# Performance work log

Measured on AMD Instinct MI355X. Metric: run time of the kernel, lower is better.

The kernel has to match this reference:

```python
import jax, jax.numpy as jnp
import numpy as np
import math

EMBED_DIM = 512
VOCAB = 96          # 95 printable ASCII + <UNK>
N_TOKENS = 16384
ALPHA = 1.5
BETA = 0.8
FRACTAL = 1.7
THETA = 0.1          # SO(4) rotation angle
LN_EPS = 1e-5        # torch LayerNorm default


def _semantic_table():
    """Faithful per-character semantic weights, L2-normalized rows. [VOCAB,4]."""
    wmap = {
        'vowels': [1.2, 0.8, 1.5, 0.9],
        'consonants': [0.9, 1.1, 0.7, 1.3],
        'digits': [1.0, 1.0, 1.0, 1.0],
        'punctuation': [0.5, 0.5, 0.8, 0.8],
        'whitespace': [0.3, 0.3, 0.3, 0.3],
        'unknown': [0.1, 0.1, 0.1, 0.1],
    }
    vocab = [chr(i) for i in range(32, 127)] + ['<UNK>']

    def cat(c):
        if c in 'aeiouAEIOU':
            return 'vowels'
        if c in 'bcdfghjklmnpqrstvwxyzBCDFGHJKLMNPQRSTVWXYZ':
            return 'consonants'
        if c in '0123456789':
            return 'digits'
        if c == ' ':
            return 'whitespace'
        if c == '<UNK>':
            return 'unknown'
        return 'punctuation'

    t = np.array([wmap[cat(c)] for c in vocab], dtype=np.float32)
    return t / np.linalg.norm(t, axis=1, keepdims=True)


def setup_inputs() -> dict:
    key = jax.random.key(0)
    k1, k2, k3, k4 = jax.random.split(key, 4)
    D, N = EMBED_DIM, N_TOKENS
    return {
        'char_idx': jax.random.randint(k1, (N,), 0, VOCAB, dtype=jnp.int32),
        'positions': jax.random.randint(k2, (N,), 0, 512, dtype=jnp.int32),
        'W': jax.random.normal(k3, (D, D), dtype=jnp.float32) * (1.0 / math.sqrt(D)),
        'b': jnp.zeros((D,), dtype=jnp.float32),
        'gamma': jnp.ones((D,), dtype=jnp.float32),
        'beta_ln': jnp.zeros((D,), dtype=jnp.float32),
        'noise': jax.random.normal(k4, (N, D), dtype=jnp.float32),  # scaled by 0.01 inside
        'sem_table': jnp.asarray(_semantic_table()),
    }


def reference(char_idx, positions, W, b, gamma, beta_ln, noise, sem_table):
    D = EMBED_DIM
    lam = char_idx.astype(jnp.float32) / VOCAB          # [N]
    t = positions.astype(jnp.float32) / 100.0           # [N]
    omega = 2.0 * math.pi * ALPHA
    kwav = 2.0 * math.pi / FRACTAL

    # Padilha wave equation (per-token complex scalars)
    ph1 = omega * t - kwav * lam + BETA * lam ** 2
    ph2 = omega * t * 1.5 - kwav * lam * 0.7 + BETA * lam ** 2 * 1.3
    a1 = jnp.sin(omega * t + ALPHA * lam)
    a2 = jnp.cos(omega * t * 0.8 + ALPHA * lam * 1.2)
    wf1 = a1 * jnp.exp(1j * ph1)                         # [N] complex64
    wf2 = a2 * jnp.exp(1j * ph2)

    i = jnp.arange(D, dtype=jnp.float32)                 # [D]
    mod1 = jnp.exp(1j * (2.0 * math.pi / D) * i[None, :] * lam[:, None])          # [N,D]
    mod2 = jnp.exp(1j * (4.0 * math.pi / D) * 1.7 * i[None, :] * lam[:, None])
    w1 = 0.6 + 0.4 * jnp.sin(0.1 * i)
    w2 = 0.4 + 0.6 * jnp.cos(0.15 * i)
    state = w1 * wf1[:, None] * mod1 + w2 * wf2[:, None] * mod2                   # [N,D] complex

    # Spectral filtering + per-token L2 normalization
    kv = jnp.arange(1, D + 1, dtype=jnp.float32)
    filt = (0.7 * jnp.exp(1j * ALPHA * jnp.arctan(jnp.log(kv + 1e-10)))
            + 0.3 * jnp.exp(1j * BETA * jnp.sin(0.1 * kv)))
    state = state * filt
    nrm = jnp.sqrt(jnp.sum(jnp.abs(state) ** 2, axis=-1, keepdims=True))
    state = state / (nrm + 1e-8)

    # SO(4) rotation, then take real part
    ct, st = math.cos(THETA), math.sin(THETA)
    x = state.real * ct - state.imag * st                # [N,D] float32

    # Adaptive linear + LayerNorm + noise
    x = x @ W.T + b
    mu = jnp.mean(x, axis=-1, keepdims=True)
    var = jnp.mean((x - mu) ** 2, axis=-1, keepdims=True)
    y = (x - mu) / jnp.sqrt(var + LN_EPS) * gamma + beta_ln + 0.01 * noise

    # Quaternion embedding
    sw = sem_table[char_idx]                             # [N,4]
    phase = (2.0 * math.pi / D) * jnp.arange(D, dtype=jnp.float32)  # [D]
    cpm = char_idx.astype(jnp.float32) * 0.01            # [N]
    q1 = y * sw[:, 0:1] * jnp.cos(phase[None, :] + cpm[:, None])
    q2 = y * sw[:, 1:2] * jnp.sin(phase[None, :] + cpm[:, None] * 1.3)
    q3 = y * sw[:, 2:3] * jnp.cos(2.0 * phase[None, :] + cpm[:, None] * 0.7)
    return jnp.stack([y, q1, q2, q3], axis=-1)           # [N,D,4]
```

## Files before the change

kernel.cpp:

```cpp
#include <hip/hip_runtime.h>
#include <math.h>

#define N_TOK 16384
#define D_DIM 512
#define PI_F 3.14159265358979323846f

typedef __bf16 bf16x8 __attribute__((ext_vector_type(8)));
typedef __bf16 bf16x4 __attribute__((ext_vector_type(4)));
typedef float floatx4 __attribute__((ext_vector_type(4)));

#define GAS __attribute__((address_space(1)))
#define LAS __attribute__((address_space(3)))

__global__ __launch_bounds__(256) void setup_kernel(
    const float* __restrict__ W, float4* __restrict__ table,
    __bf16* __restrict__ Wb) {
  const int bid = blockIdx.x;
  const int tid = threadIdx.x;
  if (bid < 96) {
    const float lam = (float)bid / 96.0f;
#pragma unroll
    for (int q = 0; q < 2; ++q) {
      const int d = tid + q * 256;
      const float fi = (float)d;
      float s1, c1, s2, c2;
      sincosf((2.0f * PI_F / 512.0f) * fi * lam, &s1, &c1);
      sincosf((4.0f * PI_F / 512.0f) * 1.7f * fi * lam, &s2, &c2);
      const float w1 = 0.6f + 0.4f * sinf(0.1f * fi);
      const float w2 = 0.4f + 0.6f * cosf(0.15f * fi);
      const float kv = fi + 1.0f;
      float fs1, fc1, fs2, fc2;
      sincosf(1.5f * atanf(logf(kv + 1e-10f)), &fs1, &fc1);
      sincosf(0.8f * sinf(0.1f * kv), &fs2, &fc2);
      const float fre = 0.7f * fc1 + 0.3f * fc2;
      const float fim = 0.7f * fs1 + 0.3f * fs2;
      table[bid * 512 + d] = make_float4(
          w1 * (c1 * fre - s1 * fim), w1 * (c1 * fim + s1 * fre),
          w2 * (c2 * fre - s2 * fim), w2 * (c2 * fim + s2 * fre));
    }
  } else {
    const int i = (bid - 96) * 256 + tid;
    const float4 w = ((const float4*)W)[i];
    bf16x4 o;
    o[0] = (__bf16)w.x; o[1] = (__bf16)w.y; o[2] = (__bf16)w.z; o[3] = (__bf16)w.w;
    ((bf16x4*)Wb)[i] = o;
  }
}

__global__ __launch_bounds__(256) void wave_kernel(
    const int* __restrict__ char_idx, const int* __restrict__ pos,
    const float4* __restrict__ table, __bf16* __restrict__ xb) {
  const int n = blockIdx.x;
  const int tid = threadIdx.x;
  const int c = char_idx[n];
  const float lam = (float)c / 96.0f;
  const float t = (float)pos[n] / 100.0f;
  const float omega = 2.0f * PI_F * 1.5f;
  const float kwav = 2.0f * PI_F / 1.7f;
  const float lam2 = lam * lam;
  float sp1, cp1, sp2, cp2;
  sincosf(omega * t - kwav * lam + 0.8f * lam2, &sp1, &cp1);
  sincosf(omega * t * 1.5f - kwav * lam * 0.7f + 1.04f * lam2, &sp2, &cp2);
  const float a1 = sinf(omega * t + 1.5f * lam);
  const float a2 = cosf(omega * t * 0.8f + 1.8f * lam);
  const float w1re = a1 * cp1, w1im = a1 * sp1;
  const float w2re = a2 * cp2, w2im = a2 * sp2;

  float zre[2], zim[2], ss = 0.0f;
#pragma unroll
  for (int q = 0; q < 2; ++q) {
    const int d = tid + q * 256;
    const float4 m = table[c * 512 + d];
    zre[q] = w1re * m.x - w1im * m.y + w2re * m.z - w2im * m.w;
    zim[q] = w1re * m.y + w1im * m.x + w2re * m.w + w2im * m.z;
    ss += zre[q] * zre[q] + zim[q] * zim[q];
  }
  __shared__ float sbuf[4];
#pragma unroll
  for (int off = 32; off > 0; off >>= 1) ss += __shfl_down(ss, off, 64);
  const int lane = tid & 63, wv = tid >> 6;
  if (lane == 0) sbuf[wv] = ss;
  __syncthreads();
  const float inv = 1.0f / (sqrtf(sbuf[0] + sbuf[1] + sbuf[2] + sbuf[3]) + 1e-8f);
  const float ct = cosf(0.1f), st = sinf(0.1f);
#pragma unroll
  for (int q = 0; q < 2; ++q) {
    xb[(size_t)n * 512 + tid + q * 256] = (__bf16)((zre[q] * ct - zim[q] * st) * inv);
  }
}

__global__ __launch_bounds__(256) void mfma_gemm(
    const __bf16* __restrict__ A, const __bf16* __restrict__ B,
    float* __restrict__ C) {
  __shared__ __align__(16) __bf16 As[128 * 32];
  __shared__ __align__(16) __bf16 Bs[128 * 32];
  const int tid = threadIdx.x;
  const int bm = blockIdx.x * 128;
  const int bn = blockIdx.y * 128;
  const int lane = tid & 63, w = tid >> 6;
  const int wm = (w >> 1) * 64, wn = (w & 1) * 64;
  const int lm = lane & 15;
  const int lk = (lane >> 4) * 8;
  const int srow = tid >> 2;
  const int skc = (tid & 3) * 8;

  floatx4 acc[4][4] = {};

  for (int kb = 0; kb < 512; kb += 32) {
    __builtin_amdgcn_global_load_lds(
        (const GAS void*)(A + (size_t)(bm + srow) * 512 + kb + skc),
        (LAS void*)(As + srow * 32 + skc), 16, 0, 0);
    __builtin_amdgcn_global_load_lds(
        (const GAS void*)(A + (size_t)(bm + 64 + srow) * 512 + kb + skc),
        (LAS void*)(As + (64 + srow) * 32 + skc), 16, 0, 0);
    __builtin_amdgcn_global_load_lds(
        (const GAS void*)(B + (size_t)(bn + srow) * 512 + kb + skc),
        (LAS void*)(Bs + srow * 32 + skc), 16, 0, 0);
    __builtin_amdgcn_global_load_lds(
        (const GAS void*)(B + (size_t)(bn + 64 + srow) * 512 + kb + skc),
        (LAS void*)(Bs + (64 + srow) * 32 + skc), 16, 0, 0);
    __syncthreads();

    bf16x8 af[4], bf[4];
#pragma unroll
    for (int i = 0; i < 4; ++i)
      af[i] = *(const bf16x8*)(As + (wm + i * 16 + lm) * 32 + lk);
#pragma unroll
    for (int j = 0; j < 4; ++j)
      bf[j] = *(const bf16x8*)(Bs + (wn + j * 16 + lm) * 32 + lk);
#pragma unroll
    for (int i = 0; i < 4; ++i)
#pragma unroll
      for (int j = 0; j < 4; ++j)
        acc[i][j] = __builtin_amdgcn_mfma_f32_16x16x32_bf16(af[i], bf[j], acc[i][j], 0, 0, 0);
    __syncthreads();
  }

  const int r0 = (lane >> 4) * 4;
#pragma unroll
  for (int i = 0; i < 4; ++i) {
    const int row = bm + wm + i * 16 + r0;
#pragma unroll
    for (int j = 0; j < 4; ++j) {
      const int col = bn + wn + j * 16 + lm;
#pragma unroll
      for (int r = 0; r < 4; ++r)
        C[(size_t)(row + r) * 512 + col] = acc[i][j][r];
    }
  }
}

__global__ __launch_bounds__(256) void epilogue_kernel(
    const float* __restrict__ xout, const int* __restrict__ char_idx,
    const float* __restrict__ b, const float* __restrict__ gamma,
    const float* __restrict__ beta_ln, const float* __restrict__ noise,
    const float* __restrict__ sem, float4* __restrict__ out) {
  const int n = blockIdx.x;
  const int tid = threadIdx.x;
  float v[2];
  v[0] = xout[(size_t)n * 512 + tid] + b[tid];
  v[1] = xout[(size_t)n * 512 + tid + 256] + b[tid + 256];
  float s = v[0] + v[1];
  float s2 = v[0] * v[0] + v[1] * v[1];
  __shared__ float sbuf[8];
#pragma unroll
  for (int off = 32; off > 0; off >>= 1) {
    s += __shfl_down(s, off, 64);
    s2 += __shfl_down(s2, off, 64);
  }
  const int lane = tid & 63, wv = tid >> 6;
  if (lane == 0) { sbuf[wv] = s; sbuf[4 + wv] = s2; }
  __syncthreads();
  const float mu = (sbuf[0] + sbuf[1] + sbuf[2] + sbuf[3]) * (1.0f / 512.0f);
  const float var = (sbuf[4] + sbuf[5] + sbuf[6] + sbuf[7]) * (1.0f / 512.0f) - mu * mu;
  const float rstd = rsqrtf(var + 1e-5f);

  const int c = char_idx[n];
  const float sw0 = sem[c * 4 + 0], sw1 = sem[c * 4 + 1], sw2 = sem[c * 4 + 2];
  const float cpm = (float)c * 0.01f;
#pragma unroll
  for (int q = 0; q < 2; ++q) {
    const int d = tid + q * 256;
    const float y = (v[q] - mu) * rstd * gamma[d] + beta_ln[d]
                    + 0.01f * noise[(size_t)n * 512 + d];
    const float ph = (2.0f * PI_F / 512.0f) * (float)d;
    const float q1 = y * sw0 * __cosf(ph + cpm);
    const float q2 = y * sw1 * __sinf(ph + cpm * 1.3f);
    const float q3 = y * sw2 * __cosf(2.0f * ph + cpm * 0.7f);
    out[(size_t)n * 512 + d] = make_float4(y, q1, q2, q3);
  }
}

extern "C" void kernel_launch(void* const* d_in, const int* in_sizes, int n_in,
                              void* d_out, int out_size, void* d_ws, size_t ws_size,
                              hipStream_t stream) {
  const int* char_idx = (const int*)d_in[0];
  const int* pos      = (const int*)d_in[1];
  const float* W      = (const float*)d_in[2];
  const float* b      = (const float*)d_in[3];
  const float* gamma  = (const float*)d_in[4];
  const float* beta_ln= (const float*)d_in[5];
  const float* noise  = (const float*)d_in[6];
  const float* sem    = (const float*)d_in[7];

  float4* table = (float4*)d_ws;
  __bf16* Wb    = (__bf16*)(table + 96 * 512);
  __bf16* xb    = Wb + 512 * 512;
  float*  xout  = (float*)(xb + (size_t)N_TOK * 512);

  setup_kernel<<<352, 256, 0, stream>>>(W, table, Wb);
  wave_kernel<<<N_TOK, 256, 0, stream>>>(char_idx, pos, table, xb);
  dim3 g2(N_TOK / 128, D_DIM / 128);
  mfma_gemm<<<g2, 256, 0, stream>>>(xb, Wb, xout);
  epilogue_kernel<<<N_TOK, 256, 0, stream>>>(xout, char_idx, b, gamma, beta_ln,
                                             noise, sem, (float4*)d_out);
}
```

Before: 220.9 us.

## Fuse wave generation, bf16 GEMM and LayerNorm epilogue into one kernel

Three kernels (wave state, MFMA GEMM, LayerNorm plus quaternion epilogue) become one kernel in which each block handles 32 tokens. The block builds the bf16 A tile in LDS, streams W from global memory with register double-buffering, and does the LayerNorm reductions and quaternion outputs directly from the accumulators. This removes the global round trips of the bf16 activations and the fp32 GEMM output. Per-row cos/sin terms are factored with angle-addition identities and fast intrinsics. In exchange every block rereads all of W (512x512 bf16), the grid is only 512 blocks, and the output and noise accesses are less coalesced.

```diff
diff --git a/kernel.cpp b/kernel.cpp
--- a/kernel.cpp
+++ b/kernel.cpp
@@ -8,9 +8,6 @@
 typedef __bf16 bf16x8 __attribute__((ext_vector_type(8)));
 typedef __bf16 bf16x4 __attribute__((ext_vector_type(4)));
 typedef float floatx4 __attribute__((ext_vector_type(4)));
-
-#define GAS __attribute__((address_space(1)))
-#define LAS __attribute__((address_space(3)))
 
 __global__ __launch_bounds__(256) void setup_kernel(
     const float* __restrict__ W, float4* __restrict__ table,
@@ -47,148 +44,163 @@
   }
 }
 
-__global__ __launch_bounds__(256) void wave_kernel(
+__global__ __launch_bounds__(256) void fused_kernel(
     const int* __restrict__ char_idx, const int* __restrict__ pos,
-    const float4* __restrict__ table, __bf16* __restrict__ xb) {
-  const int n = blockIdx.x;
-  const int tid = threadIdx.x;
-  const int c = char_idx[n];
-  const float lam = (float)c / 96.0f;
-  const float t = (float)pos[n] / 100.0f;
-  const float omega = 2.0f * PI_F * 1.5f;
-  const float kwav = 2.0f * PI_F / 1.7f;
-  const float lam2 = lam * lam;
-  float sp1, cp1, sp2, cp2;
-  sincosf(omega * t - kwav * lam + 0.8f * lam2, &sp1, &cp1);
-  sincosf(omega * t * 1.5f - kwav * lam * 0.7f + 1.04f * lam2, &sp2, &cp2);
-  const float a1 = sinf(omega * t + 1.5f * lam);
-  const float a2 = cosf(omega * t * 0.8f + 1.8f * lam);
-  const float w1re = a1 * cp1, w1im = a1 * sp1;
-  const float w2re = a2 * cp2, w2im = a2 * sp2;
-
-  float zre[2], zim[2], ss = 0.0f;
-#pragma unroll
-  for (int q = 0; q < 2; ++q) {
-    const int d = tid + q * 256;
-    const float4 m = table[c * 512 + d];
-    zre[q] = w1re * m.x - w1im * m.y + w2re * m.z - w2im * m.w;
-    zim[q] = w1re * m.y + w1im * m.x + w2re * m.w + w2im * m.z;
-    ss += zre[q] * zre[q] + zim[q] * zim[q];
-  }
-  __shared__ float sbuf[4];
-#pragma unroll
-  for (int off = 32; off > 0; off >>= 1) ss += __shfl_down(ss, off, 64);
-  const int lane = tid & 63, wv = tid >> 6;
-  if (lane == 0) sbuf[wv] = ss;
-  __syncthreads();
-  const float inv = 1.0f / (sqrtf(sbuf[0] + sbuf[1] + sbuf[2] + sbuf[3]) + 1e-8f);
-  const float ct = cosf(0.1f), st = sinf(0.1f);
-#pragma unroll
-  for (int q = 0; q < 2; ++q) {
-    xb[(size_t)n * 512 + tid + q * 256] = (__bf16)((zre[q] * ct - zim[q] * st) * inv);
-  }
-}
-
-__global__ __launch_bounds__(256) void mfma_gemm(
-    const __bf16* __restrict__ A, const __bf16* __restrict__ B,
-    float* __restrict__ C) {
-  __shared__ __align__(16) __bf16 As[128 * 32];
-  __shared__ __align__(16) __bf16 Bs[128 * 32];
-  const int tid = threadIdx.x;
-  const int bm = blockIdx.x * 128;
-  const int bn = blockIdx.y * 128;
-  const int lane = tid & 63, w = tid >> 6;
-  const int wm = (w >> 1) * 64, wn = (w & 1) * 64;
-  const int lm = lane & 15;
-  const int lk = (lane >> 4) * 8;
-  const int srow = tid >> 2;
-  const int skc = (tid & 3) * 8;
-
-  floatx4 acc[4][4] = {};
-
-  for (int kb = 0; kb < 512; kb += 32) {
-    __builtin_amdgcn_global_load_lds(
-        (const GAS void*)(A + (size_t)(bm + srow) * 512 + kb + skc),
-        (LAS void*)(As + srow * 32 + skc), 16, 0, 0);
-    __builtin_amdgcn_global_load_lds(
-        (const GAS void*)(A + (size_t)(bm + 64 + srow) * 512 + kb + skc),
-        (LAS void*)(As + (64 + srow) * 32 + skc), 16, 0, 0);
-    __builtin_amdgcn_global_load_lds(
-        (const GAS void*)(B + (size_t)(bn + srow) * 512 + kb + skc),
-        (LAS void*)(Bs + srow * 32 + skc), 16, 0, 0);
-    __builtin_amdgcn_global_load_lds(
-        (const GAS void*)(B + (size_t)(bn + 64 + srow) * 512 + kb + skc),
-        (LAS void*)(Bs + (64 + srow) * 32 + skc), 16, 0, 0);
-    __syncthreads();
-
-    bf16x8 af[4], bf[4];
-#pragma unroll
-    for (int i = 0; i < 4; ++i)
-      af[i] = *(const bf16x8*)(As + (wm + i * 16 + lm) * 32 + lk);
-#pragma unroll
-    for (int j = 0; j < 4; ++j)
-      bf[j] = *(const bf16x8*)(Bs + (wn + j * 16 + lm) * 32 + lk);
-#pragma unroll
-    for (int i = 0; i < 4; ++i)
-#pragma unroll
-      for (int j = 0; j < 4; ++j)
-        acc[i][j] = __builtin_amdgcn_mfma_f32_16x16x32_bf16(af[i], bf[j], acc[i][j], 0, 0, 0);
-    __syncthreads();
-  }
-
-  const int r0 = (lane >> 4) * 4;
-#pragma unroll
-  for (int i = 0; i < 4; ++i) {
-    const int row = bm + wm + i * 16 + r0;
-#pragma unroll
-    for (int j = 0; j < 4; ++j) {
-      const int col = bn + wn + j * 16 + lm;
-#pragma unroll
-      for (int r = 0; r < 4; ++r)
-        C[(size_t)(row + r) * 512 + col] = acc[i][j][r];
-    }
-  }
-}
-
-__global__ __launch_bounds__(256) void epilogue_kernel(
-    const float* __restrict__ xout, const int* __restrict__ char_idx,
+    const float4* __restrict__ table, const __bf16* __restrict__ Wb,
     const float* __restrict__ b, const float* __restrict__ gamma,
     const float* __restrict__ beta_ln, const float* __restrict__ noise,
     const float* __restrict__ sem, float4* __restrict__ out) {
-  const int n = blockIdx.x;
+  __shared__ __align__(16) __bf16 A_lds[16 * 2 * 64 * 8];
+  __shared__ float2 rc1[32], rc2[32], rc3[32];
+  __shared__ float part[4][32][2];
+  __shared__ float stats[32][2];
+
   const int tid = threadIdx.x;
-  float v[2];
-  v[0] = xout[(size_t)n * 512 + tid] + b[tid];
-  v[1] = xout[(size_t)n * 512 + tid + 256] + b[tid + 256];
-  float s = v[0] + v[1];
-  float s2 = v[0] * v[0] + v[1] * v[1];
-  __shared__ float sbuf[8];
-#pragma unroll
-  for (int off = 32; off > 0; off >>= 1) {
-    s += __shfl_down(s, off, 64);
-    s2 += __shfl_down(s2, off, 64);
-  }
-  const int lane = tid & 63, wv = tid >> 6;
-  if (lane == 0) { sbuf[wv] = s; sbuf[4 + wv] = s2; }
+  const int lane = tid & 63, w = tid >> 6;
+  const int row0 = blockIdx.x * 32;
+  const float ct = 0.99500416527f, st = 0.09983341664f;
+
+  for (int rr = 0; rr < 8; ++rr) {
+    const int m = w * 8 + rr;
+    const int n = row0 + m;
+    const int c = char_idx[n];
+    const float lam = (float)c * (1.0f / 96.0f);
+    const float t = (float)pos[n] * 0.01f;
+    const float omega = 2.0f * PI_F * 1.5f;
+    const float kwav = 2.0f * PI_F / 1.7f;
+    const float lam2 = lam * lam;
+    float sp1, cp1, sp2, cp2;
+    __sincosf(omega * t - kwav * lam + 0.8f * lam2, &sp1, &cp1);
+    __sincosf(omega * t * 1.5f - kwav * lam * 0.7f + 1.04f * lam2, &sp2, &cp2);
+    const float a1 = __sinf(omega * t + 1.5f * lam);
+    const float a2 = __cosf(omega * t * 0.8f + 1.8f * lam);
+    const float w1re = a1 * cp1, w1im = a1 * sp1;
+    const float w2re = a2 * cp2, w2im = a2 * sp2;
+
+    const float4* tp = table + c * 512 + lane * 8;
+    float zre[8], zim[8], ss = 0.0f;
+#pragma unroll
+    for (int j = 0; j < 8; ++j) {
+      const float4 mm = tp[j];
+      zre[j] = w1re * mm.x - w1im * mm.y + w2re * mm.z - w2im * mm.w;
+      zim[j] = w1re * mm.y + w1im * mm.x + w2re * mm.w + w2im * mm.z;
+      ss += zre[j] * zre[j] + zim[j] * zim[j];
+    }
+#pragma unroll
+    for (int off = 32; off > 0; off >>= 1) ss += __shfl_down(ss, off, 64);
+    ss = __shfl(ss, 0, 64);
+    const float inv = 1.0f / (sqrtf(ss) + 1e-8f);
+    bf16x8 av;
+#pragma unroll
+    for (int j = 0; j < 8; ++j) av[j] = (__bf16)((zre[j] * ct - zim[j] * st) * inv);
+    const int kc = lane >> 2, prt = lane & 3, mt = m >> 4;
+    *(bf16x8*)(A_lds + (((kc * 2 + mt) * 64) + ((prt << 4) | (m & 15))) * 8) = av;
+
+    if (lane == 0) {
+      const float cpm = (float)c * 0.01f;
+      float s, cc;
+      __sincosf(cpm, &s, &cc);
+      rc1[m] = make_float2(sem[c * 4 + 0] * cc, sem[c * 4 + 0] * s);
+      __sincosf(cpm * 1.3f, &s, &cc);
+      rc2[m] = make_float2(sem[c * 4 + 1] * cc, sem[c * 4 + 1] * s);
+      __sincosf(cpm * 0.7f, &s, &cc);
+      rc3[m] = make_float2(sem[c * 4 + 2] * cc, sem[c * 4 + 2] * s);
+    }
+  }
   __syncthreads();
-  const float mu = (sbuf[0] + sbuf[1] + sbuf[2] + sbuf[3]) * (1.0f / 512.0f);
-  const float var = (sbuf[4] + sbuf[5] + sbuf[6] + sbuf[7]) * (1.0f / 512.0f) - mu * mu;
-  const float rstd = rsqrtf(var + 1e-5f);
-
-  const int c = char_idx[n];
-  const float sw0 = sem[c * 4 + 0], sw1 = sem[c * 4 + 1], sw2 = sem[c * 4 + 2];
-  const float cpm = (float)c * 0.01f;
-#pragma unroll
-  for (int q = 0; q < 2; ++q) {
-    const int d = tid + q * 256;
-    const float y = (v[q] - mu) * rstd * gamma[d] + beta_ln[d]
-                    + 0.01f * noise[(size_t)n * 512 + d];
-    const float ph = (2.0f * PI_F / 512.0f) * (float)d;
-    const float q1 = y * sw0 * __cosf(ph + cpm);
-    const float q2 = y * sw1 * __sinf(ph + cpm * 1.3f);
-    const float q3 = y * sw2 * __cosf(2.0f * ph + cpm * 0.7f);
-    out[(size_t)n * 512 + d] = make_float4(y, q1, q2, q3);
-  }
+
+  const int cl = lane & 15, kq = lane >> 4;
+  const int wn = w * 128;
+  const __bf16* Bbase = Wb + (size_t)(wn + cl) * 512 + kq * 8;
+  floatx4 acc[2][8] = {};
+  bf16x8 bcur[8], bnxt[8];
+#pragma unroll
+  for (int j = 0; j < 8; ++j) bcur[j] = *(const bf16x8*)(Bbase + j * 16 * 512);
+  for (int kc = 0; kc < 16; ++kc) {
+    if (kc < 15) {
+#pragma unroll
+      for (int j = 0; j < 8; ++j)
+        bnxt[j] = *(const bf16x8*)(Bbase + j * 16 * 512 + (kc + 1) * 32);
+    }
+    const bf16x8 a0 = *(const bf16x8*)(A_lds + ((kc * 2 + 0) * 64 + lane) * 8);
+    const bf16x8 a1 = *(const bf16x8*)(A_lds + ((kc * 2 + 1) * 64 + lane) * 8);
+#pragma unroll
+    for (int j = 0; j < 8; ++j) {
+      acc[0][j] = __builtin_amdgcn_mfma_f32_16x16x32_bf16(a0, bcur[j], acc[0][j], 0, 0, 0);
+      acc[1][j] = __builtin_amdgcn_mfma_f32_16x16x32_bf16(a1, bcur[j], acc[1][j], 0, 0, 0);
+    }
+#pragma unroll
+    for (int j = 0; j < 8; ++j) bcur[j] = bnxt[j];
+  }
+
+  float bj[8], gj[8], btj[8], cph[8], sph[8];
+#pragma unroll
+  for (int j = 0; j < 8; ++j) {
+    const int col = wn + j * 16 + cl;
+    bj[j] = b[col]; gj[j] = gamma[col]; btj[j] = beta_ln[col];
+    __sincosf((2.0f * PI_F / 512.0f) * (float)col, &sph[j], &cph[j]);
+  }
+  float ps[8] = {}, ps2[8] = {};
+#pragma unroll
+  for (int i = 0; i < 2; ++i)
+#pragma unroll
+    for (int j = 0; j < 8; ++j)
+#pragma unroll
+      for (int r = 0; r < 4; ++r) {
+        const float v = acc[i][j][r] + bj[j];
+        acc[i][j][r] = v;
+        ps[i * 4 + r] += v;
+        ps2[i * 4 + r] += v * v;
+      }
+#pragma unroll
+  for (int mask = 1; mask < 16; mask <<= 1)
+#pragma unroll
+    for (int tt = 0; tt < 8; ++tt) {
+      ps[tt] += __shfl_xor(ps[tt], mask, 64);
+      ps2[tt] += __shfl_xor(ps2[tt], mask, 64);
+    }
+  if (cl == 0) {
+#pragma unroll
+    for (int i = 0; i < 2; ++i)
+#pragma unroll
+      for (int r = 0; r < 4; ++r) {
+        const int m = i * 16 + kq * 4 + r;
+        part[w][m][0] = ps[i * 4 + r];
+        part[w][m][1] = ps2[i * 4 + r];
+      }
+  }
+  __syncthreads();
+  if (tid < 32) {
+    const float s = part[0][tid][0] + part[1][tid][0] + part[2][tid][0] + part[3][tid][0];
+    const float s2 = part[0][tid][1] + part[1][tid][1] + part[2][tid][1] + part[3][tid][1];
+    const float mu = s * (1.0f / 512.0f);
+    const float var = s2 * (1.0f / 512.0f) - mu * mu;
+    stats[tid][0] = mu;
+    stats[tid][1] = rsqrtf(var + 1e-5f);
+  }
+  __syncthreads();
+
+#pragma unroll
+  for (int i = 0; i < 2; ++i)
+#pragma unroll
+    for (int r = 0; r < 4; ++r) {
+      const int m = i * 16 + kq * 4 + r;
+      const float mu = stats[m][0], rstd = stats[m][1];
+      const float2 c1 = rc1[m], c2 = rc2[m], c3 = rc3[m];
+      const size_t rowoff = (size_t)(row0 + m) * 512;
+#pragma unroll
+      for (int j = 0; j < 8; ++j) {
+        const int col = wn + j * 16 + cl;
+        const float y = (acc[i][j][r] - mu) * rstd * gj[j] + btj[j]
+                        + 0.01f * noise[rowoff + col];
+        const float c2p = cph[j] * cph[j] - sph[j] * sph[j];
+        const float s2p = 2.0f * sph[j] * cph[j];
+        const float q1 = y * (c1.x * cph[j] - c1.y * sph[j]);
+        const float q2 = y * (c2.x * sph[j] + c2.y * cph[j]);
+        const float q3 = y * (c3.x * c2p - c3.y * s2p);
+        out[rowoff + col] = make_float4(y, q1, q2, q3);
+      }
+    }
 }
 
 extern "C" void kernel_launch(void* const* d_in, const int* in_sizes, int n_in,
@@ -205,13 +217,9 @@
 
   float4* table = (float4*)d_ws;
   __bf16* Wb    = (__bf16*)(table + 96 * 512);
-  __bf16* xb    = Wb + 512 * 512;
-  float*  xout  = (float*)(xb + (size_t)N_TOK * 512);
 
   setup_kernel<<<352, 256, 0, stream>>>(W, table, Wb);
-  wave_kernel<<<N_TOK, 256, 0, stream>>>(char_idx, pos, table, xb);
-  dim3 g2(N_TOK / 128, D_DIM / 128);
-  mfma_gemm<<<g2, 256, 0, stream>>>(xb, Wb, xout);
-  epilogue_kernel<<<N_TOK, 256, 0, stream>>>(xout, char_idx, b, gamma, beta_ln,
-                                             noise, sem, (float4*)d_out);
+  fused_kernel<<<N_TOK / 32, 256, 0, stream>>>(char_idx, pos, table, Wb, b,
+                                               gamma, beta_ln, noise, sem,
+                                               (float4*)d_out);
 }
```

After: 247.3 us. +11.9%, slower.
